# Kernel tuning notes

Hardware: AMD Instinct MI355X
Metric: run time of the kernel (lower is better)

Reference implementation:

```python
import jax, jax.numpy as jnp
import numpy as np

# Static hyperparams matching init_kwargs
KSIZE, STRIDE, PAD, DIL = 3, 2, 1, 1


def setup_inputs() -> dict:
    key = jax.random.key(0)
    k1, k2 = jax.random.split(key)
    B, H, W, Cin, Cout = 8, 128, 128, 128, 256
    feats = jax.random.normal(k1, (B * H * W, Cin), dtype=jnp.float32)
    weight = jax.random.normal(k2, (KSIZE * KSIZE, Cin, Cout), dtype=jnp.float32) * 0.05
    alpha_upper = jnp.ones((1,), dtype=jnp.float32)
    # dense grid coords [N, 3] = (batch, y, x), matching a dense image sparse tensor
    bb, yy, xx = np.meshgrid(np.arange(B), np.arange(H), np.arange(W), indexing='ij')
    coords = jnp.asarray(np.stack([bb, yy, xx], -1).reshape(-1, 3), dtype=jnp.int32)
    return {"feats": feats, "weight": weight, "alpha_upper": alpha_upper,
            "coords": coords, "H": H, "W": W, "B": B}


def _coord_ranges(H, W):
    # Faithful translation of WrappedMinkowskiStridedOperation.__init__ + forward
    # coordinate math, specialized to a dense grid (per-batch min=0, max=H-1/W-1).
    kernel_origin = DIL * ((KSIZE - 1) // 2) * (KSIZE % 2)
    dilated = DIL * (KSIZE - 1) + 1
    ks_off = kernel_origin - dilated + 1          # _kernel_start_offset
    ke_off = kernel_origin                        # _kernel_end_offset
    idx_start = kernel_origin - PAD               # _index_start_offset
    ranges = []
    for ext in (H, W):
        idx_end = (ext - 1) + kernel_origin + PAD - dilated + 2
        start = max(idx_start, (0 + ks_off - idx_start) // STRIDE * STRIDE + idx_start)
        end = min(idx_end, ((ext - 1 + ke_off - idx_start) // STRIDE + 1) * STRIDE + idx_start)
        ranges.append(np.arange(start, end, STRIDE))
    offsets = np.arange(KSIZE) * DIL - kernel_origin  # kernel region offsets
    return ranges[0], ranges[1], offsets, idx_start


def reference(feats, weight, alpha_upper, coords, H, W, B):
    Cin = feats.shape[1]
    Cout = weight.shape[-1]
    ys, xs, offs, idx_start = _coord_ranges(H, W)
    OH, OW = len(ys), len(xs)
    oy, ox = jnp.meshgrid(jnp.asarray(ys, jnp.int32), jnp.asarray(xs, jnp.int32), indexing='ij')
    dy, dx = np.meshgrid(offs, offs, indexing='ij')
    dy = jnp.asarray(dy.reshape(-1), jnp.int32)  # [kvol]
    dx = jnp.asarray(dx.reshape(-1), jnp.int32)
    ny = oy[None] + dy[:, None, None]            # [kvol, OH, OW]
    nx = ox[None] + dx[:, None, None]
    valid = (ny >= 0) & (ny < H) & (nx >= 0) & (nx < W)
    lin = jnp.clip(ny, 0, H - 1) * W + jnp.clip(nx, 0, W - 1)  # [kvol, OH, OW]
    feats3 = feats.reshape(B, H * W, Cin)
    gathered = feats3[:, lin]                    # [B, kvol, OH, OW, Cin]
    gathered = jnp.where(valid[None, ..., None], gathered, jnp.zeros((), feats.dtype))
    out = jnp.einsum('bkhwc,kcd->bhwd', gathered, weight)  # [B, OH, OW, Cout]
    out_feats = out.reshape(B * OH * OW, Cout)
    # output coordinates, remapped as in forward (shift by index_start, divide by stride)
    oc = jnp.stack([oy, ox], -1).reshape(-1, 2)  # [OH*OW, 2]
    oc = (oc - jnp.int32(idx_start)) // jnp.int32(STRIDE)
    oc = jnp.tile(oc, (B, 1))
    bcol = jnp.repeat(jnp.arange(B, dtype=jnp.int32), OH * OW)
    out_coords = jnp.concatenate([bcol[:, None], oc], axis=1)
    return out_feats, out_coords, alpha_upper
```

## Files before the change

kernel.cpp:

```cpp
#include <hip/hip_runtime.h>


#define OUT_FEATS_ELEMS (32768 * 256)
#define OUT_COORDS_OFF  OUT_FEATS_ELEMS
#define ALPHA_OFF       (OUT_FEATS_ELEMS + 32768 * 3)

#define BW_BYTES   (18 * 16384)

typedef float v16f __attribute__((ext_vector_type(16)));

__device__ __forceinline__ unsigned pk4fp8(float a, float b, float c, float d) {
    unsigned u = 0;
    u = __builtin_amdgcn_cvt_pk_fp8_f32(a, b, u, false);
    u = __builtin_amdgcn_cvt_pk_fp8_f32(c, d, u, true);
    return u;
}

#define GLOAD_LDS16(SRC, DST)                                                  \
    __builtin_amdgcn_global_load_lds(                                          \
        (const __attribute__((address_space(1))) void*)(SRC),                  \
        (__attribute__((address_space(3))) void*)(DST), 16, 0, 0)

__global__ void wprep_kernel(const float* __restrict__ w,
                             const float* __restrict__ alpha,
                             unsigned char* __restrict__ Bw,
                             float* __restrict__ out) {
    int cid = blockIdx.x * 256 + threadIdx.x;
    if (cid < 32768) {
        int b = cid >> 12, iy = (cid >> 6) & 63, ix = cid & 63;
        float* c = out + OUT_COORDS_OFF + (size_t)cid * 3;
        c[0] = (float)b; c[1] = (float)iy; c[2] = (float)ix;
        if (cid == 0) out[ALPHA_OFF] = alpha[0];
    }
    if (cid < 18432) {
        int ch  = cid & 7;
        int row = (cid >> 3) & 127;
        int t   = cid >> 10;
        int nb  = (t >= 9) ? 1 : 0;
        int tap = t - 9 * nb;
        int chp = ch ^ (row & 7);
        int n   = (nb << 7) + row;
        int kb  = (tap << 7) + (chp << 4);
        unsigned u[4];
#pragma unroll
        for (int q = 0; q < 4; ++q) {
            float f0 = w[(size_t)(kb + 4 * q + 0) * 256 + n];
            float f1 = w[(size_t)(kb + 4 * q + 1) * 256 + n];
            float f2 = w[(size_t)(kb + 4 * q + 2) * 256 + n];
            float f3 = w[(size_t)(kb + 4 * q + 3) * 256 + n];
            u[q] = pk4fp8(f0, f1, f2, f3);
        }
        uint4 r; r.x = u[0]; r.y = u[1]; r.z = u[2]; r.w = u[3];
        *(uint4*)(Bw + (size_t)cid * 16) = r;
    }
}

__global__ void coords_alpha_kernel(float* __restrict__ out, const float* __restrict__ alpha) {
    int i = blockIdx.x * 256 + threadIdx.x;
    int b = i >> 12, iy = (i >> 6) & 63, ix = i & 63;
    float* c = out + OUT_COORDS_OFF + (size_t)i * 3;
    c[0] = (float)b; c[1] = (float)iy; c[2] = (float)ix;
    if (i == 0) out[ALPHA_OFF] = alpha[0];
}

__global__ __launch_bounds__(1024, 1) void gemm_conv_kernel(
    const float* __restrict__ feats,
    const unsigned char* __restrict__ Bw,
    float* __restrict__ out)
{
    __shared__ unsigned char Aband[5 * 130 * 128];
    __shared__ unsigned char Bs[2][256 * 128];

    const int tid  = threadIdx.x;
    const int bid  = blockIdx.x;
    const int my   = ((bid & 7) << 5) + (bid >> 3);
    const int m0   = my << 7;
    const int bb   = my >> 5;
    const int iy0  = ((my & 31) << 1);

    const int lane = tid & 63, wave = tid >> 6;
    const int wm   = (wave >> 2) << 5;
    const int wn   = (wave & 3) << 6;
    const int l31  = lane & 31;
    const int hh   = lane >> 5;
    const int xorl = l31 & 7;

    const unsigned char* bsrc0 = Bw + ((size_t)((wave >> 3) * 9) << 14)
                                    + ((size_t)(wave & 7) << 11) + ((size_t)lane << 4);
    auto stageB = [&](int tap, int buf) {
        const unsigned char* bs = bsrc0 + ((size_t)tap << 14);
        unsigned char* bdst = Bs[buf] + (wave << 11);
#pragma unroll
        for (int q = 0; q < 2; ++q)
            GLOAD_LDS16(bs + (q << 10), bdst + (q << 10));
    };

    stageB(0, 0);

    if (tid < 40) {
        const int r = tid >> 3, c = tid & 7;
        uint4 z; z.x = 0u; z.y = 0u; z.z = 0u; z.w = 0u;
        *(uint4*)(Aband + ((r * 130) << 7) + (c << 4)) = z;
    }
    if (iy0 == 0) {
        for (int z = tid; z < 1040; z += 1024) {
            const int nxp = z >> 3, c = z & 7;
            uint4 zz; zz.x = 0u; zz.y = 0u; zz.z = 0u; zz.w = 0u;
            *(uint4*)(Aband + (nxp << 7) + ((c ^ ((nxp >> 1) & 7)) << 4)) = zz;
        }
    }

    {
        const int ny0 = (iy0 << 1) - 1;
        auto loadBand = [&](int vstart, int iters) {
#pragma unroll 4
            for (int it = 0; it < iters; ++it) {
                const int o   = (tid + (it << 10)) << 4;
                const int r   = vstart + (o >> 16);
                const int br  = o & 65535;
                const int nx  = br >> 9;
                const int ch0 = (br & 511) >> 2;
                const float4 f = *(const float4*)(feats +
                    ((((size_t)(bb << 14) + (ny0 + r) * 128 + nx)) << 7) + ch0);
                const unsigned u = pk4fp8(f.x, f.y, f.z, f.w);
                const int c   = ch0 >> 4;
                const int nxp = nx + 1;
                *(unsigned*)(Aband + ((r * 130 + nxp) << 7)
                             + ((c ^ ((nxp >> 1) & 7)) << 4) + (ch0 & 15)) = u;
            }
        };
        if (iy0 == 0) loadBand(1, 16); else loadBand(0, 20);
    }
    __syncthreads();

    v16f acc[2];
#pragma unroll
    for (int j = 0; j < 2; j++) acc[j] = (v16f)(0.0f);

    auto computeTap = [&](int buf, int dy, int dx) {
        const int bandrow = ((wm >> 6) << 1) + dy + 1;
        const int ixv = (wm & 63) + l31;
        const int nxp = (ixv << 1) + dx + 1;
        const int abase = ((bandrow * 130 + nxp) << 7) + (hh << 3);
        const int akey  = (nxp >> 1) & 7;
#pragma unroll
        for (int seg = 0; seg < 8; ++seg) {
            long long a0, b2[2];
            a0 = *(const long long*)(Aband + abase + ((seg ^ akey) << 4));
#pragma unroll
            for (int j = 0; j < 2; j++)
                b2[j] = *(const long long*)(Bs[buf] + ((wn + (j << 5) + l31) << 7)
                                            + ((seg ^ xorl) << 4) + (hh << 3));
            __builtin_amdgcn_s_setprio(1);
#pragma unroll
            for (int j = 0; j < 2; j++)
                acc[j] = __builtin_amdgcn_mfma_f32_32x32x16_fp8_fp8(a0, b2[j], acc[j], 0, 0, 0);
            __builtin_amdgcn_s_setprio(0);
        }
    };

#pragma unroll
    for (int tap = 0; tap < 9; ++tap) {
        if (tap < 8) {
            stageB(tap + 1, (tap + 1) & 1);
            asm volatile("s_waitcnt vmcnt(2)\ns_barrier" ::: "memory");
        } else {
            asm volatile("s_waitcnt vmcnt(0)\ns_barrier" ::: "memory");
        }
        computeTap(tap & 1, tap / 3 - 1, tap % 3 - 1);
        if (tap < 8)
            asm volatile("s_barrier" ::: "memory");
    }

#pragma unroll
    for (int j = 0; j < 2; j++) {
        const int gcol = wn + (j << 5) + l31;
#pragma unroll
        for (int r = 0; r < 16; ++r) {
            const int grow = m0 + wm + (r & 3) + ((r >> 2) << 3) + (hh << 2);
            __builtin_nontemporal_store(acc[j][r], &out[(size_t)grow * 256 + gcol]);
        }
    }
}

__global__ void naive_conv_kernel(const float* __restrict__ feats,
                                  const float* __restrict__ w,
                                  float* __restrict__ out) {
    int m = blockIdx.x;
    int n = threadIdx.x;
    int bb = m >> 12, iy = (m >> 6) & 63, ix = m & 63;
    float acc = 0.f;
    for (int tap = 0; tap < 9; ++tap) {
        int ny = 2 * iy + tap / 3 - 1;
        int nx = 2 * ix + tap % 3 - 1;
        if ((unsigned)ny < 128u && (unsigned)nx < 128u) {
            const float* fr = feats + ((size_t)((bb << 14) + (ny << 7) + nx) << 7);
            const float* wr = w + tap * 32768 + n;
            for (int c = 0; c < 128; ++c) acc += fr[c] * wr[c * 256];
        }
    }
    out[(size_t)m * 256 + n] = acc;
}

extern "C" void kernel_launch(void* const* d_in, const int* in_sizes, int n_in,
                              void* d_out, int out_size, void* d_ws, size_t ws_size,
                              hipStream_t stream) {
    const float* feats  = (const float*)d_in[0];
    const float* weight = (const float*)d_in[1];
    const float* alpha  = (const float*)d_in[2];
    float* out = (float*)d_out;

    const size_t NEED = (size_t)BW_BYTES;
    if (ws_size >= NEED) {
        unsigned char* Bw = (unsigned char*)d_ws;
        wprep_kernel<<<144, 256, 0, stream>>>(weight, alpha, Bw, out);
        gemm_conv_kernel<<<256, 1024, 0, stream>>>(feats, Bw, out);
    } else {
        coords_alpha_kernel<<<128, 256, 0, stream>>>(out, alpha);
        naive_conv_kernel<<<32768, 256, 0, stream>>>(feats, weight, out);
    }
}
```

Baseline: 132.7 us.

## Retile conv GEMM into smaller 64x128 blocks with N-split and more occupancy

Replaces the 256-block, 1024-thread tiling (128 output rows x 256 channels per block) with 1024 blocks of 512 threads, each computing one output row (64 pixels) for half the output channels. The A band shrinks to 3 input rows without explicit left padding, and the padded column is handled by zeroing the fragment in registers. Smaller LDS footprint and launch bounds of 4 blocks per CU aim to raise occupancy and fill all CUs better. The cost is that each block now re-reads and re-converts its input band for both channel halves, so feature loads and fp8 conversions double, and each wave holds a single accumulator with less B reuse.

Result: slower. 145.1 us (+9.3%).

```diff
diff --git a/kernel.cpp b/kernel.cpp
--- a/kernel.cpp
+++ b/kernel.cpp
@@ -63,30 +63,32 @@
     if (i == 0) out[ALPHA_OFF] = alpha[0];
 }
 
-__global__ __launch_bounds__(1024, 1) void gemm_conv_kernel(
+__global__ __launch_bounds__(512, 4) void gemm_conv_kernel(
     const float* __restrict__ feats,
     const unsigned char* __restrict__ Bw,
     float* __restrict__ out)
 {
-    __shared__ unsigned char Aband[5 * 130 * 128];
-    __shared__ unsigned char Bs[2][256 * 128];
+    __shared__ unsigned char Aband[3 * 128 * 128];
+    __shared__ unsigned char Bs[2][128 * 128];
 
     const int tid  = threadIdx.x;
     const int bid  = blockIdx.x;
-    const int my   = ((bid & 7) << 5) + (bid >> 3);
-    const int m0   = my << 7;
-    const int bb   = my >> 5;
-    const int iy0  = ((my & 31) << 1);
+    const int my   = ((bid & 7) << 6) + ((bid >> 3) & 63);
+    const int nb   = bid >> 9;
+    const int m0   = my << 6;
+    const int n0   = nb << 7;
+    const int bb   = my >> 6;
+    const int iy   = my & 63;
 
     const int lane = tid & 63, wave = tid >> 6;
     const int wm   = (wave >> 2) << 5;
-    const int wn   = (wave & 3) << 6;
+    const int wn   = (wave & 3) << 5;
     const int l31  = lane & 31;
     const int hh   = lane >> 5;
     const int xorl = l31 & 7;
 
-    const unsigned char* bsrc0 = Bw + ((size_t)((wave >> 3) * 9) << 14)
-                                    + ((size_t)(wave & 7) << 11) + ((size_t)lane << 4);
+    const unsigned char* bsrc0 = Bw + ((size_t)(nb * 9) << 14)
+                                    + ((size_t)wave << 11) + ((size_t)lane << 4);
     auto stageB = [&](int tap, int buf) {
         const unsigned char* bs = bsrc0 + ((size_t)tap << 14);
         unsigned char* bdst = Bs[buf] + (wave << 11);
@@ -97,25 +99,20 @@
 
     stageB(0, 0);
 
-    if (tid < 40) {
-        const int r = tid >> 3, c = tid & 7;
-        uint4 z; z.x = 0u; z.y = 0u; z.z = 0u; z.w = 0u;
-        *(uint4*)(Aband + ((r * 130) << 7) + (c << 4)) = z;
-    }
-    if (iy0 == 0) {
-        for (int z = tid; z < 1040; z += 1024) {
-            const int nxp = z >> 3, c = z & 7;
+    if (iy == 0) {
+        for (int z = tid; z < 1024; z += 512) {
+            const int nx = z >> 3, c = z & 7;
             uint4 zz; zz.x = 0u; zz.y = 0u; zz.z = 0u; zz.w = 0u;
-            *(uint4*)(Aband + (nxp << 7) + ((c ^ ((nxp >> 1) & 7)) << 4)) = zz;
+            *(uint4*)(Aband + (nx << 7) + ((c ^ (((nx + 1) >> 1) & 7)) << 4)) = zz;
         }
     }
 
     {
-        const int ny0 = (iy0 << 1) - 1;
+        const int ny0 = (iy << 1) - 1;
         auto loadBand = [&](int vstart, int iters) {
 #pragma unroll 4
             for (int it = 0; it < iters; ++it) {
-                const int o   = (tid + (it << 10)) << 4;
+                const int o   = (tid + (it << 9)) << 4;
                 const int r   = vstart + (o >> 16);
                 const int br  = o & 65535;
                 const int nx  = br >> 9;
@@ -123,38 +120,33 @@
                 const float4 f = *(const float4*)(feats +
                     ((((size_t)(bb << 14) + (ny0 + r) * 128 + nx)) << 7) + ch0);
                 const unsigned u = pk4fp8(f.x, f.y, f.z, f.w);
-                const int c   = ch0 >> 4;
-                const int nxp = nx + 1;
-                *(unsigned*)(Aband + ((r * 130 + nxp) << 7)
-                             + ((c ^ ((nxp >> 1) & 7)) << 4) + (ch0 & 15)) = u;
+                const int c = ch0 >> 4;
+                *(unsigned*)(Aband + ((r * 128 + nx) << 7)
+                             + ((c ^ (((nx + 1) >> 1) & 7)) << 4) + (ch0 & 15)) = u;
             }
         };
-        if (iy0 == 0) loadBand(1, 16); else loadBand(0, 20);
+        if (iy == 0) loadBand(1, 16); else loadBand(0, 24);
     }
     __syncthreads();
 
-    v16f acc[2];
-#pragma unroll
-    for (int j = 0; j < 2; j++) acc[j] = (v16f)(0.0f);
+    v16f acc = (v16f)(0.0f);
 
     auto computeTap = [&](int buf, int dy, int dx) {
-        const int bandrow = ((wm >> 6) << 1) + dy + 1;
-        const int ixv = (wm & 63) + l31;
-        const int nxp = (ixv << 1) + dx + 1;
-        const int abase = ((bandrow * 130 + nxp) << 7) + (hh << 3);
-        const int akey  = (nxp >> 1) & 7;
+        const int r   = dy + 1;
+        const int ixv = wm + l31;
+        const int nxq = (ixv << 1) + dx;
+        const bool pad = (nxq < 0);
+        const int nxs = pad ? 0 : nxq;
+        const int abase = ((r << 7) + nxs) << 7;
+        const int akey  = ((nxq + 1) >> 1) & 7;
 #pragma unroll
         for (int seg = 0; seg < 8; ++seg) {
-            long long a0, b2[2];
-            a0 = *(const long long*)(Aband + abase + ((seg ^ akey) << 4));
-#pragma unroll
-            for (int j = 0; j < 2; j++)
-                b2[j] = *(const long long*)(Bs[buf] + ((wn + (j << 5) + l31) << 7)
-                                            + ((seg ^ xorl) << 4) + (hh << 3));
+            long long a0 = *(const long long*)(Aband + abase + ((seg ^ akey) << 4) + (hh << 3));
+            if (pad) a0 = 0LL;
+            long long b0 = *(const long long*)(Bs[buf] + ((wn + l31) << 7)
+                                               + ((seg ^ xorl) << 4) + (hh << 3));
             __builtin_amdgcn_s_setprio(1);
-#pragma unroll
-            for (int j = 0; j < 2; j++)
-                acc[j] = __builtin_amdgcn_mfma_f32_32x32x16_fp8_fp8(a0, b2[j], acc[j], 0, 0, 0);
+            acc = __builtin_amdgcn_mfma_f32_32x32x16_fp8_fp8(a0, b0, acc, 0, 0, 0);
             __builtin_amdgcn_s_setprio(0);
         }
     };
@@ -172,13 +164,12 @@
             asm volatile("s_barrier" ::: "memory");
     }
 
-#pragma unroll
-    for (int j = 0; j < 2; j++) {
-        const int gcol = wn + (j << 5) + l31;
+    {
+        const int gcol = n0 + wn + l31;
 #pragma unroll
         for (int r = 0; r < 16; ++r) {
             const int grow = m0 + wm + (r & 3) + ((r >> 2) << 3) + (hh << 2);
-            __builtin_nontemporal_store(acc[j][r], &out[(size_t)grow * 256 + gcol]);
+            __builtin_nontemporal_store(acc[r], &out[(size_t)grow * 256 + gcol]);
         }
     }
 }
@@ -214,7 +205,7 @@
     if (ws_size >= NEED) {
         unsigned char* Bw = (unsigned char*)d_ws;
         wprep_kernel<<<144, 256, 0, stream>>>(weight, alpha, Bw, out);
-        gemm_conv_kernel<<<256, 1024, 0, stream>>>(feats, Bw, out);
+        gemm_conv_kernel<<<1024, 512, 0, stream>>>(feats, Bw, out);
     } else {
         coords_alpha_kernel<<<128, 256, 0, stream>>>(out, alpha);
         naive_conv_kernel<<<32768, 256, 0, stream>>>(feats, weight, out);
```
